# Kernel tuning notes

Measured on AMD Instinct MI355X. Metric: run time of the kernel, lower is better.

Reference implementation:

```python
import jax, jax.numpy as jnp
import numpy as np

N = 100000      # nodes
D = 128         # input feature dim
K = 8           # propagation hops (concat K+1 blocks)
HID = 512
OUT = 32
E = 1600000     # edges (avg degree 16)
BN_EPS = 1e-5
DEG_EPS = 1e-8


def setup_inputs() -> dict:
    key = jax.random.key(0)
    ks = jax.random.split(key, 8)
    feature = jax.random.normal(ks[0], (N, D), dtype=jnp.float32)
    coor = jax.random.uniform(ks[1], (N, 2), dtype=jnp.float32)
    edge_index = jax.random.randint(ks[2], (2, E), 0, N, dtype=jnp.int32)
    theta = jnp.array(1.0, dtype=jnp.float32)  # Gaussian bandwidth param
    fan1 = D * (K + 1)
    W1 = jax.random.normal(ks[3], (HID, fan1), dtype=jnp.float32) * (1.0 / np.sqrt(fan1))
    b1 = jnp.zeros((HID,), dtype=jnp.float32)
    gamma = jnp.ones((HID,), dtype=jnp.float32)
    beta = jnp.zeros((HID,), dtype=jnp.float32)
    W2 = jax.random.normal(ks[4], (OUT, HID), dtype=jnp.float32) * (1.0 / np.sqrt(HID))
    b2 = jnp.zeros((OUT,), dtype=jnp.float32)
    return {"feature": feature, "coor": coor, "theta": theta,
            "W1": W1, "b1": b1, "gamma": gamma, "beta": beta,
            "W2": W2, "b2": b2, "edge_index": edge_index, "m": 1}


def reference(feature, coor, theta, W1, b1, gamma, beta, W2, b2, edge_index, m):
    row, col = edge_index[0], edge_index[1]  # dst, src
    # Gaussian kernel edge weights from coordinate distances (gather on coor)
    diff = coor[row] - coor[col]                       # [E, 2]
    dist2 = jnp.sum(diff * diff, axis=-1)              # [E]
    w = jnp.exp(-dist2 * theta / m)                    # [E]
    # degree (row) normalization via scatter-add
    deg = jax.ops.segment_sum(w, row, num_segments=N)  # [N]
    norm = w / (deg[row] + DEG_EPS)                    # [E]
    # K sequential propagations, concat with input (-> N x D*(K+1))
    xs = [feature]
    x = feature
    for _ in range(K):
        msgs = x[col] * norm[:, None]                  # [E, D] gather + weight
        x = jax.ops.segment_sum(msgs, row, num_segments=N)  # [N, D] scatter
        xs.append(x)
    h = jnp.concatenate(xs, axis=-1)                   # [N, D*(K+1)]
    # MLP head: fc1 -> leaky_relu(0.2) -> BatchNorm1d (batch stats) -> fc2
    h = jax.nn.leaky_relu(h @ W1.T + b1, negative_slope=0.2)
    mu = jnp.mean(h, axis=0)
    var = jnp.var(h, axis=0)
    h = (h - mu) * jax.lax.rsqrt(var + BN_EPS) * gamma + beta
    # dropout omitted (deterministic/eval reference)
    return h @ W2.T + b2
```

## Files before the change

kernel.cpp:

```cpp
#include <hip/hip_runtime.h>
#include <hip/hip_bf16.h>
#include <cstdint>
#include <cstddef>

#define NNODES 100000
#define DFEAT 128
#define KHOP 8
#define FAN1 1152
#define HIDN 512
#define OUTD 32
#define NEDGE 1600000
#define BN_EPS 1e-5f
#define DEG_EPS 1e-8f

using short8 = __attribute__((ext_vector_type(8))) short;
using f32x4  = __attribute__((ext_vector_type(4))) float;

__device__ __forceinline__ float bf16lo(uint32_t u) { return __uint_as_float(u << 16); }
__device__ __forceinline__ float bf16hi(uint32_t u) { return __uint_as_float(u & 0xffff0000u); }
__device__ __forceinline__ float bf16s(short x) {
    return __uint_as_float(((uint32_t)(uint16_t)x) << 16);
}
__device__ __forceinline__ uint32_t packbf(float a, float b) {
    uint32_t lo = __bfloat16_as_ushort(__float2bfloat16(a));
    uint32_t hi = __bfloat16_as_ushort(__float2bfloat16(b));
    return lo | (hi << 16);
}

__device__ __forceinline__ void gload16(const void* g, void* l) {
    __builtin_amdgcn_global_load_lds(
        (const __attribute__((address_space(1))) uint32_t*)g,
        (__attribute__((address_space(3))) uint32_t*)l, 16, 0, 0);
}

struct Blk3 { const __hip_bfloat16* p[3]; };

__global__ __launch_bounds__(256) void edge_kernel(
    const int* __restrict__ ei, const float* __restrict__ coor,
    const float* __restrict__ theta, const int* __restrict__ mm,
    float* __restrict__ deg, int* __restrict__ cnt)
{
    int e = blockIdx.x * 256 + threadIdx.x;
    if (e >= NEDGE) return;
    float tom = theta[0] / (float)mm[0];
    int r = ei[e], c = ei[NEDGE + e];
    float2 pr = *(const float2*)(coor + 2*(size_t)r);
    float2 pc = *(const float2*)(coor + 2*(size_t)c);
    float dx = pr.x - pc.x, dy = pr.y - pc.y;
    float w = expf(-(dx*dx + dy*dy) * tom);
    atomicAdd(&deg[r], w);
    atomicAdd(&cnt[r], 1);
}

__global__ __launch_bounds__(1024) void scan_local(
    const int* __restrict__ cnt, int* __restrict__ row_ptr,
    int* __restrict__ bsum, int n)
{
    __shared__ int wsum[16];
    int b = blockIdx.x, tid = threadIdx.x;
    int i = b * 1024 + tid;
    int lane = tid & 63, wv = tid >> 6;
    int v = (i < n) ? cnt[i] : 0;
    #pragma unroll
    for (int off = 1; off < 64; off <<= 1) {
        int t = __shfl_up(v, off, 64);
        if (lane >= off) v += t;
    }
    if (lane == 63) wsum[wv] = v;
    __syncthreads();
    if (tid < 16) {
        int t = wsum[tid];
        #pragma unroll
        for (int off = 1; off < 16; off <<= 1) {
            int u = __shfl_up(t, off, 64);
            if (tid >= off) t += u;
        }
        wsum[tid] = t;
    }
    __syncthreads();
    int incl = v + ((wv == 0) ? 0 : wsum[wv - 1]);
    if (i < n) row_ptr[i + 1] = incl;
    if (tid == 0) bsum[b] = wsum[15];
}

__global__ __launch_bounds__(128) void scan_carry(int* __restrict__ bsum, int n)
{
    __shared__ int ws[2];
    int tid = threadIdx.x, lane = tid & 63, wv = tid >> 6;
    int v = (tid < n) ? bsum[tid] : 0;
    int incl = v;
    #pragma unroll
    for (int off = 1; off < 64; off <<= 1) {
        int t = __shfl_up(incl, off, 64);
        if (lane >= off) incl += t;
    }
    if (lane == 63) ws[wv] = incl;
    __syncthreads();
    int excl = incl - v + ((wv == 0) ? 0 : ws[0]);
    if (tid < n) bsum[tid] = excl;
}

__global__ __launch_bounds__(256) void scan_add(
    const int* __restrict__ bsum, int* __restrict__ row_ptr, int n)
{
    int i = blockIdx.x * 256 + threadIdx.x;
    if (i == 0) row_ptr[0] = 0;
    if (i < n) row_ptr[i + 1] += bsum[i >> 10];
}

__global__ __launch_bounds__(256) void fill_kernel(
    const int* __restrict__ ei, const float* __restrict__ coor,
    const float* __restrict__ theta, const int* __restrict__ mm,
    const float* __restrict__ deg, const int* __restrict__ row_ptr,
    int* __restrict__ fill, int* __restrict__ cols, float* __restrict__ nrm)
{
    int e = blockIdx.x * 256 + threadIdx.x;
    if (e >= NEDGE) return;
    float tom = theta[0] / (float)mm[0];
    int r = ei[e], c = ei[NEDGE + e];
    float2 pr = *(const float2*)(coor + 2*(size_t)r);
    float2 pc = *(const float2*)(coor + 2*(size_t)c);
    float dx = pr.x - pc.x, dy = pr.y - pc.y;
    float w = expf(-(dx*dx + dy*dy) * tom);
    int pos = row_ptr[r] + atomicAdd(&fill[r], 1);
    cols[pos] = c;
    nrm[pos] = w / (deg[r] + DEG_EPS);
}

__global__ __launch_bounds__(256) void cast_feat_kernel(
    const float* __restrict__ f, __hip_bfloat16* __restrict__ x0)
{
    int i = blockIdx.x * 256 + threadIdx.x;
    int node = i >> 6, l2 = i & 63;
    if (node >= NNODES) return;
    float2 v = *(const float2*)(f + (size_t)node * DFEAT + l2 * 2);
    __hip_bfloat162 hb;
    hb.x = __float2bfloat16(v.x);
    hb.y = __float2bfloat16(v.y);
    *(__hip_bfloat162*)(x0 + (size_t)node * DFEAT + l2 * 2) = hb;
}

__global__ __launch_bounds__(256) void cast_w1_kernel(
    const float* __restrict__ w1, __hip_bfloat16* __restrict__ o)
{
    int i = blockIdx.x * 256 + threadIdx.x;
    if (i < HIDN * FAN1) o[i] = __float2bfloat16(w1[i]);
}

__global__ __launch_bounds__(256) void prop_kernel(
    const __hip_bfloat16* __restrict__ x, __hip_bfloat16* __restrict__ y,
    const int* __restrict__ row_ptr, const int* __restrict__ cols,
    const float* __restrict__ nrm)
{
    int gw = (blockIdx.x * 256 + threadIdx.x) >> 6;
    if (gw >= NNODES) return;
    int lane = threadIdx.x & 63;
    int q = lane >> 4, sl = lane & 15;
    int beg = row_ptr[gw], end = row_ptr[gw + 1];
    float a0 = 0.f, a1 = 0.f, a2 = 0.f, a3 = 0.f;
    float a4 = 0.f, a5 = 0.f, a6 = 0.f, a7 = 0.f;
    int e = beg + q;
    for (; e + 12 < end; e += 16) {
        int s0 = cols[e], s1 = cols[e + 4], s2 = cols[e + 8], s3 = cols[e + 12];
        float w0 = nrm[e], w1 = nrm[e + 4], w2 = nrm[e + 8], w3 = nrm[e + 12];
        uint4 u0 = *(const uint4*)(x + (size_t)s0 * DFEAT + sl * 8);
        uint4 u1 = *(const uint4*)(x + (size_t)s1 * DFEAT + sl * 8);
        uint4 u2 = *(const uint4*)(x + (size_t)s2 * DFEAT + sl * 8);
        uint4 u3 = *(const uint4*)(x + (size_t)s3 * DFEAT + sl * 8);
        a0 += w0 * bf16lo(u0.x); a1 += w0 * bf16hi(u0.x);
        a2 += w0 * bf16lo(u0.y); a3 += w0 * bf16hi(u0.y);
        a4 += w0 * bf16lo(u0.z); a5 += w0 * bf16hi(u0.z);
        a6 += w0 * bf16lo(u0.w); a7 += w0 * bf16hi(u0.w);
        a0 += w1 * bf16lo(u1.x); a1 += w1 * bf16hi(u1.x);
        a2 += w1 * bf16lo(u1.y); a3 += w1 * bf16hi(u1.y);
        a4 += w1 * bf16lo(u1.z); a5 += w1 * bf16hi(u1.z);
        a6 += w1 * bf16lo(u1.w); a7 += w1 * bf16hi(u1.w);
        a0 += w2 * bf16lo(u2.x); a1 += w2 * bf16hi(u2.x);
        a2 += w2 * bf16lo(u2.y); a3 += w2 * bf16hi(u2.y);
        a4 += w2 * bf16lo(u2.z); a5 += w2 * bf16hi(u2.z);
        a6 += w2 * bf16lo(u2.w); a7 += w2 * bf16hi(u2.w);
        a0 += w3 * bf16lo(u3.x); a1 += w3 * bf16hi(u3.x);
        a2 += w3 * bf16lo(u3.y); a3 += w3 * bf16hi(u3.y);
        a4 += w3 * bf16lo(u3.z); a5 += w3 * bf16hi(u3.z);
        a6 += w3 * bf16lo(u3.w); a7 += w3 * bf16hi(u3.w);
    }
    for (; e < end; e += 4) {
        int s0 = cols[e];
        float w0 = nrm[e];
        uint4 u0 = *(const uint4*)(x + (size_t)s0 * DFEAT + sl * 8);
        a0 += w0 * bf16lo(u0.x); a1 += w0 * bf16hi(u0.x);
        a2 += w0 * bf16lo(u0.y); a3 += w0 * bf16hi(u0.y);
        a4 += w0 * bf16lo(u0.z); a5 += w0 * bf16hi(u0.z);
        a6 += w0 * bf16lo(u0.w); a7 += w0 * bf16hi(u0.w);
    }
    a0 += __shfl_xor(a0, 16, 64); a0 += __shfl_xor(a0, 32, 64);
    a1 += __shfl_xor(a1, 16, 64); a1 += __shfl_xor(a1, 32, 64);
    a2 += __shfl_xor(a2, 16, 64); a2 += __shfl_xor(a2, 32, 64);
    a3 += __shfl_xor(a3, 16, 64); a3 += __shfl_xor(a3, 32, 64);
    a4 += __shfl_xor(a4, 16, 64); a4 += __shfl_xor(a4, 32, 64);
    a5 += __shfl_xor(a5, 16, 64); a5 += __shfl_xor(a5, 32, 64);
    a6 += __shfl_xor(a6, 16, 64); a6 += __shfl_xor(a6, 32, 64);
    a7 += __shfl_xor(a7, 16, 64); a7 += __shfl_xor(a7, 32, 64);
    if (q == 0) {
        uint4 o;
        o.x = packbf(a0, a1);
        o.y = packbf(a2, a3);
        o.z = packbf(a4, a5);
        o.w = packbf(a6, a7);
        *(uint4*)(y + (size_t)gw * DFEAT + sl * 8) = o;
    }
}

__global__ __launch_bounds__(256) void fc1_kernel(
    Blk3 blks, const __hip_bfloat16* __restrict__ w1,
    const float* __restrict__ b1, __hip_bfloat16* __restrict__ h1b,
    float* __restrict__ gsum, float* __restrict__ gsq,
    int nkt, int kb0, int mode)
{
    __shared__ char smem[33792];
    int pid = blockIdx.x;
    int lid = (pid & 7) * 391 + (pid >> 3);
    int n0 = (lid & 3) * 128;
    int m0 = (lid >> 2) * 128;
    int tid = threadIdx.x, lane = tid & 63, wv = tid >> 6;
    int wr = wv >> 1, wc = wv & 1;

    f32x4 acc[4][4];
    #pragma unroll
    for (int i = 0; i < 4; ++i)
        #pragma unroll
        for (int j = 0; j < 4; ++j)
            acc[i][j] = (f32x4){0.f, 0.f, 0.f, 0.f};

#define STAGE(hb, ktv) do {                                                   \
        const __hip_bfloat16* xp = blks.p[(ktv) >> 2];                        \
        int koff_ = ((ktv) & 3) * 32;                                         \
        int kglob_ = (kb0 + ((ktv) >> 2)) * 128 + koff_;                      \
        char* Ab_ = smem + (hb) * 16384;                                      \
        char* Bb_ = Ab_ + 8192;                                               \
        _Pragma("unroll")                                                     \
        for (int l = 0; l < 2; ++l) {                                         \
            int u = l * 256 + wv * 64 + lane;                                 \
            int row_ = u >> 2, qq_ = u & 3;                                   \
            gload16(xp + (size_t)(m0 + row_) * DFEAT + koff_ + qq_ * 8,       \
                    Ab_ + u * 16);                                            \
            gload16(w1 + (size_t)(n0 + row_) * FAN1 + kglob_ + qq_ * 8,       \
                    Bb_ + u * 16);                                            \
        }                                                                     \
    } while (0)

    STAGE(0, 0);
    for (int kt = 0; kt < nkt; ++kt) {
        int cur = kt & 1;
        __builtin_amdgcn_s_barrier();
        if (kt + 1 < nkt) {
            STAGE(cur ^ 1, kt + 1);
            asm volatile("s_waitcnt vmcnt(4)" ::: "memory");
        } else {
            asm volatile("s_waitcnt vmcnt(0)" ::: "memory");
        }
        __builtin_amdgcn_s_barrier();
        char* Ab = smem + cur * 16384;
        char* Bb = Ab + 8192;
        short8 af[4], bfr[4];
        #pragma unroll
        for (int i = 0; i < 4; ++i)
            af[i] = *(const short8*)(Ab + (wr * 64 + i * 16 + (lane & 15)) * 64 + (lane >> 4) * 16);
        #pragma unroll
        for (int j = 0; j < 4; ++j)
            bfr[j] = *(const short8*)(Bb + (wc * 64 + j * 16 + (lane & 15)) * 64 + (lane >> 4) * 16);
        #pragma unroll
        for (int j = 0; j < 4; ++j)
            #pragma unroll
            for (int i = 0; i < 4; ++i)
                acc[i][j] = __builtin_amdgcn_mfma_f32_16x16x32_bf16(af[i], bfr[j], acc[i][j], 0, 0, 0);
    }
#undef STAGE

    __syncthreads();
    __hip_bfloat16* tile = (__hip_bfloat16*)smem;
    float* lsum = (float*)(smem + 32768);
    float* lsq  = lsum + 128;
    bool fin = (mode & 2) != 0;
    if (fin && tid < 128) { lsum[tid] = 0.f; lsq[tid] = 0.f; }
    #pragma unroll
    for (int i = 0; i < 4; ++i) {
        #pragma unroll
        for (int j = 0; j < 4; ++j) {
            int col = wc * 64 + j * 16 + (lane & 15);
            #pragma unroll
            for (int r = 0; r < 4; ++r) {
                int row = wr * 64 + i * 16 + (lane >> 4) * 4 + r;
                tile[row * 128 + col] = __float2bfloat16(acc[i][j][r]);
            }
        }
    }
    __syncthreads();

    int cu = tid & 15, tr = tid >> 4;
    float bias[8];
    float s[8], q[8];
    #pragma unroll
    for (int e = 0; e < 8; ++e) { s[e] = 0.f; q[e] = 0.f; }
    if (fin) {
        #pragma unroll
        for (int e = 0; e < 8; ++e) bias[e] = b1[n0 + cu * 8 + e];
    }
    size_t blkbase = (size_t)(n0 >> 7) * NNODES * 128;
    for (int p = 0; p < 8; ++p) {
        int row = p * 16 + tr;
        int gm = m0 + row;
        if (gm >= NNODES) continue;
        short8 fresh = *(const short8*)(tile + row * 128 + cu * 8);
        size_t gidx = blkbase + (size_t)gm * 128 + cu * 8;
        float v[8];
        #pragma unroll
        for (int e = 0; e < 8; ++e) v[e] = bf16s(fresh[e]);
        if (mode & 1) {
            short8 prev = *(const short8*)(h1b + gidx);
            #pragma unroll
            for (int e = 0; e < 8; ++e) v[e] += bf16s(prev[e]);
        }
        if (fin) {
            #pragma unroll
            for (int e = 0; e < 8; ++e) {
                float t = v[e] + bias[e];
                t = (t > 0.f) ? t : 0.2f * t;
                v[e] = t;
                s[e] += t;
                q[e] += t * t;
            }
        }
        short8 outv;
        #pragma unroll
        for (int e = 0; e < 8; ++e) outv[e] = (short)__bfloat16_as_ushort(__float2bfloat16(v[e]));
        *(short8*)(h1b + gidx) = outv;
    }
    if (fin) {
        #pragma unroll
        for (int e = 0; e < 8; ++e) {
            atomicAdd(&lsum[cu * 8 + e], s[e]);
            atomicAdd(&lsq[cu * 8 + e], q[e]);
        }
        __syncthreads();
        if (tid < 128) {
            atomicAdd(&gsum[n0 + tid], lsum[tid]);
            atomicAdd(&gsq[n0 + tid], lsq[tid]);
        }
    }
}

__global__ __launch_bounds__(512) void bn_finalize(
    const float* __restrict__ gsum, const float* __restrict__ gsq,
    const float* __restrict__ gamma, const float* __restrict__ beta,
    const float* __restrict__ w2, const float* __restrict__ b2,
    __hip_bfloat16* __restrict__ w2s, float* __restrict__ cvec)
{
    __shared__ float ts[HIDN];
    int tid = threadIdx.x;
    float mu = gsum[tid] * (1.0f / NNODES);
    float var = gsq[tid] * (1.0f / NNODES) - mu * mu;
    float s = gamma[tid] * rsqrtf(var + BN_EPS);
    float t = beta[tid] - mu * s;
    ts[tid] = t;
    for (int o = 0; o < OUTD; ++o)
        w2s[o * HIDN + tid] = __float2bfloat16(w2[o * HIDN + tid] * s);
    __syncthreads();
    int lane = tid & 63, wv = tid >> 6;
    for (int o = wv; o < OUTD; o += 8) {
        float p = 0.f;
        for (int j = lane; j < HIDN; j += 64) p += ts[j] * w2[o * HIDN + j];
        #pragma unroll
        for (int off = 32; off; off >>= 1) p += __shfl_xor(p, off, 64);
        if (lane == 0) cvec[o] = p + b2[o];
    }
}

__global__ __launch_bounds__(256) void fc2_kernel(
    const __hip_bfloat16* __restrict__ h1b, const __hip_bfloat16* __restrict__ w2s,
    const float* __restrict__ cvec, float* __restrict__ out)
{
    int gw = (blockIdx.x * 256 + threadIdx.x) >> 6;
    if (gw >= NNODES / 16) return;
    int lane = threadIdx.x & 63;
    int m0 = gw * 16;
    f32x4 acc[2];
    acc[0] = (f32x4){0.f, 0.f, 0.f, 0.f};
    acc[1] = (f32x4){0.f, 0.f, 0.f, 0.f};
    #pragma unroll
    for (int kt = 0; kt < HIDN / 32; ++kt) {
        int k0 = kt * 32;
        short8 a = *(const short8*)(h1b
            + ((size_t)(kt >> 2) * NNODES + (m0 + (lane & 15))) * 128
            + (kt & 3) * 32 + (lane >> 4) * 8);
        #pragma unroll
        for (int j = 0; j < 2; ++j) {
            short8 b = *(const short8*)(w2s + (size_t)(j * 16 + (lane & 15)) * HIDN + k0 + (lane >> 4) * 8);
            acc[j] = __builtin_amdgcn_mfma_f32_16x16x32_bf16(a, b, acc[j], 0, 0, 0);
        }
    }
    #pragma unroll
    for (int j = 0; j < 2; ++j) {
        int col = j * 16 + (lane & 15);
        float cadd = cvec[col];
        #pragma unroll
        for (int r = 0; r < 4; ++r) {
            int row = m0 + (lane >> 4) * 4 + r;
            out[(size_t)row * OUTD + col] = acc[j][r] + cadd;
        }
    }
}

struct Ptrs {
    float *deg, *nrm, *gsum, *gsq, *cvec;
    int *cnt, *fillc, *row_ptr, *colsb, *bsum;
    __hip_bfloat16 *slot[3], *h1acc, *w1b, *w2s;
};

static size_t layout(char* base, Ptrs& P) {
    char* p = base;
    auto take = [&](size_t b) {
        char* q = (char*)(((uintptr_t)p + 255) & ~(uintptr_t)255);
        p = q + b;
        return q;
    };
    P.deg     = (float*)take((size_t)NNODES * 4);
    P.cnt     = (int*)  take((size_t)NNODES * 4);
    P.fillc   = (int*)  take((size_t)NNODES * 4);
    P.row_ptr = (int*)  take((size_t)(NNODES + 1) * 4);
    P.bsum    = (int*)  take(128 * 4);
    P.colsb   = (int*)  take((size_t)NEDGE * 4);
    P.nrm     = (float*)take((size_t)NEDGE * 4);
    P.h1acc   = (__hip_bfloat16*)take((size_t)NNODES * HIDN * 2 + 65536);
    P.w1b     = (__hip_bfloat16*)take((size_t)HIDN * FAN1 * 2);
    P.w2s     = (__hip_bfloat16*)take((size_t)OUTD * HIDN * 2);
    P.gsum    = (float*)take(HIDN * 4);
    P.gsq     = (float*)take(HIDN * 4);
    P.cvec    = (float*)take(OUTD * 4);
    for (int i = 0; i < 3; ++i)
        P.slot[i] = (__hip_bfloat16*)take((size_t)NNODES * DFEAT * 2 + 32768);
    return (size_t)(p - base);
}

extern "C" void kernel_launch(void* const* d_in, const int* in_sizes, int n_in,
                              void* d_out, int out_size, void* d_ws, size_t ws_size,
                              hipStream_t stream)
{
    const float* feature = (const float*)d_in[0];
    const float* coor    = (const float*)d_in[1];
    const float* theta   = (const float*)d_in[2];
    const float* W1      = (const float*)d_in[3];
    const float* b1      = (const float*)d_in[4];
    const float* gamma   = (const float*)d_in[5];
    const float* beta    = (const float*)d_in[6];
    const float* W2      = (const float*)d_in[7];
    const float* b2      = (const float*)d_in[8];
    const int*   ei      = (const int*)d_in[9];
    const int*   mm      = (const int*)d_in[10];
    float* out = (float*)d_out;
    (void)in_sizes; (void)n_in; (void)out_size; (void)ws_size;

    Ptrs P;
    layout((char*)d_ws, P);

    hipMemsetAsync(P.deg,   0, (size_t)NNODES * 4, stream);
    hipMemsetAsync(P.cnt,   0, (size_t)NNODES * 4, stream);
    hipMemsetAsync(P.fillc, 0, (size_t)NNODES * 4, stream);
    hipMemsetAsync(P.gsum,  0, HIDN * 4, stream);
    hipMemsetAsync(P.gsq,   0, HIDN * 4, stream);

    int eb = (NEDGE + 255) / 256;
    int nchunk = (NNODES + 1023) / 1024;
    edge_kernel<<<eb, 256, 0, stream>>>(ei, coor, theta, mm, P.deg, P.cnt);
    scan_local<<<nchunk, 1024, 0, stream>>>(P.cnt, P.row_ptr, P.bsum, NNODES);
    scan_carry<<<1, 128, 0, stream>>>(P.bsum, nchunk);
    scan_add<<<(NNODES + 255) / 256, 256, 0, stream>>>(P.bsum, P.row_ptr, NNODES);
    fill_kernel<<<eb, 256, 0, stream>>>(ei, coor, theta, mm, P.deg, P.row_ptr,
                                        P.fillc, P.colsb, P.nrm);

    cast_w1_kernel<<<(HIDN * FAN1 + 255) / 256, 256, 0, stream>>>(W1, P.w1b);
    cast_feat_kernel<<<(NNODES * 64) / 256, 256, 0, stream>>>(feature, P.slot[0]);

    int pb = (NNODES * 64) / 256;
    int fgrid = 8 * 391;

    auto launch_fc1 = [&](int kb0, int mode) {
        Blk3 b;
        for (int i = 0; i < 3; ++i) b.p[i] = P.slot[i];
        fc1_kernel<<<fgrid, 256, 0, stream>>>(b, P.w1b, b1, P.h1acc,
                                              P.gsum, P.gsq, 12, kb0, mode);
    };

    for (int k = 1; k <= KHOP; ++k) {
        prop_kernel<<<pb, 256, 0, stream>>>(P.slot[(k - 1) % 3],
                                            P.slot[k % 3],
                                            P.row_ptr, P.colsb, P.nrm);
        if (k == 2) launch_fc1(0, 0);
        if (k == 5) launch_fc1(3, 1);
    }
    launch_fc1(6, 3);

    bn_finalize<<<1, 512, 0, stream>>>(P.gsum, P.gsq, gamma, beta, W2, b2,
                                       P.w2s, P.cvec);
    fc2_kernel<<<(NNODES / 16 * 64 + 255) / 256, 256, 0, stream>>>(P.h1acc, P.w2s,
                                                                   P.cvec, out);
}
```

Measured before the change: 1.030 ms.

## Pack degree and count into one 64-bit atomic, record per-edge rank, interleave CSR edges

The separate float degree and int count atomics are merged into a single 64-bit atomicAdd that holds a fixed-point weight sum in the low 48 bits and the edge count in the high bits. The returned old count becomes a per-edge rank, so the fill pass no longer needs a second atomic counter or its memset. Column index and normalized weight are stored interleaved as a uint2, so the propagation kernel issues one 8-byte load per edge instead of two 4-byte loads. In exchange, degree becomes fixed-point (2^26 scale), which loses some precision, and the 16-bit rank assumes no node has more than 65535 in-edges.

```diff
diff --git a/kernel.cpp b/kernel.cpp
--- a/kernel.cpp
+++ b/kernel.cpp
@@ -12,6 +12,7 @@
 #define NEDGE 1600000
 #define BN_EPS 1e-5f
 #define DEG_EPS 1e-8f
+#define FIXSCALE 67108864.0f
 
 using short8 = __attribute__((ext_vector_type(8))) short;
 using f32x4  = __attribute__((ext_vector_type(4))) float;
@@ -38,7 +39,7 @@
 __global__ __launch_bounds__(256) void edge_kernel(
     const int* __restrict__ ei, const float* __restrict__ coor,
     const float* __restrict__ theta, const int* __restrict__ mm,
-    float* __restrict__ deg, int* __restrict__ cnt)
+    unsigned long long* __restrict__ packed, unsigned short* __restrict__ rank)
 {
     int e = blockIdx.x * 256 + threadIdx.x;
     if (e >= NEDGE) return;
@@ -48,19 +49,21 @@
     float2 pc = *(const float2*)(coor + 2*(size_t)c);
     float dx = pr.x - pc.x, dy = pr.y - pc.y;
     float w = expf(-(dx*dx + dy*dy) * tom);
-    atomicAdd(&deg[r], w);
-    atomicAdd(&cnt[r], 1);
+    unsigned long long enc = (1ULL << 48)
+        | (unsigned long long)(unsigned int)__float2uint_rn(w * FIXSCALE);
+    unsigned long long old = atomicAdd(&packed[r], enc);
+    rank[e] = (unsigned short)(old >> 48);
 }
 
 __global__ __launch_bounds__(1024) void scan_local(
-    const int* __restrict__ cnt, int* __restrict__ row_ptr,
+    const unsigned long long* __restrict__ packed, int* __restrict__ row_ptr,
     int* __restrict__ bsum, int n)
 {
     __shared__ int wsum[16];
     int b = blockIdx.x, tid = threadIdx.x;
     int i = b * 1024 + tid;
     int lane = tid & 63, wv = tid >> 6;
-    int v = (i < n) ? cnt[i] : 0;
+    int v = (i < n) ? (int)(packed[i] >> 48) : 0;
     #pragma unroll
     for (int off = 1; off < 64; off <<= 1) {
         int t = __shfl_up(v, off, 64);
@@ -111,8 +114,9 @@
 __global__ __launch_bounds__(256) void fill_kernel(
     const int* __restrict__ ei, const float* __restrict__ coor,
     const float* __restrict__ theta, const int* __restrict__ mm,
-    const float* __restrict__ deg, const int* __restrict__ row_ptr,
-    int* __restrict__ fill, int* __restrict__ cols, float* __restrict__ nrm)
+    const unsigned long long* __restrict__ packed,
+    const unsigned short* __restrict__ rank, const int* __restrict__ row_ptr,
+    uint2* __restrict__ edat)
 {
     int e = blockIdx.x * 256 + threadIdx.x;
     if (e >= NEDGE) return;
@@ -122,9 +126,12 @@
     float2 pc = *(const float2*)(coor + 2*(size_t)c);
     float dx = pr.x - pc.x, dy = pr.y - pc.y;
     float w = expf(-(dx*dx + dy*dy) * tom);
-    int pos = row_ptr[r] + atomicAdd(&fill[r], 1);
-    cols[pos] = c;
-    nrm[pos] = w / (deg[r] + DEG_EPS);
+    float deg = (float)(double)(packed[r] & 0xFFFFFFFFFFFFULL) * (1.0f / FIXSCALE);
+    int pos = row_ptr[r] + rank[e];
+    uint2 d;
+    d.x = (unsigned)c;
+    d.y = __float_as_uint(w / (deg + DEG_EPS));
+    edat[pos] = d;
 }
 
 __global__ __launch_bounds__(256) void cast_feat_kernel(
@@ -149,8 +156,7 @@
 
 __global__ __launch_bounds__(256) void prop_kernel(
     const __hip_bfloat16* __restrict__ x, __hip_bfloat16* __restrict__ y,
-    const int* __restrict__ row_ptr, const int* __restrict__ cols,
-    const float* __restrict__ nrm)
+    const int* __restrict__ row_ptr, const uint2* __restrict__ edat)
 {
     int gw = (blockIdx.x * 256 + threadIdx.x) >> 6;
     if (gw >= NNODES) return;
@@ -161,12 +167,13 @@
     float a4 = 0.f, a5 = 0.f, a6 = 0.f, a7 = 0.f;
     int e = beg + q;
     for (; e + 12 < end; e += 16) {
-        int s0 = cols[e], s1 = cols[e + 4], s2 = cols[e + 8], s3 = cols[e + 12];
-        float w0 = nrm[e], w1 = nrm[e + 4], w2 = nrm[e + 8], w3 = nrm[e + 12];
-        uint4 u0 = *(const uint4*)(x + (size_t)s0 * DFEAT + sl * 8);
-        uint4 u1 = *(const uint4*)(x + (size_t)s1 * DFEAT + sl * 8);
-        uint4 u2 = *(const uint4*)(x + (size_t)s2 * DFEAT + sl * 8);
-        uint4 u3 = *(const uint4*)(x + (size_t)s3 * DFEAT + sl * 8);
+        uint2 e0 = edat[e], e1 = edat[e + 4], e2 = edat[e + 8], e3 = edat[e + 12];
+        float w0 = __uint_as_float(e0.y), w1 = __uint_as_float(e1.y);
+        float w2 = __uint_as_float(e2.y), w3 = __uint_as_float(e3.y);
+        uint4 u0 = *(const uint4*)(x + (size_t)e0.x * DFEAT + sl * 8);
+        uint4 u1 = *(const uint4*)(x + (size_t)e1.x * DFEAT + sl * 8);
+        uint4 u2 = *(const uint4*)(x + (size_t)e2.x * DFEAT + sl * 8);
+        uint4 u3 = *(const uint4*)(x + (size_t)e3.x * DFEAT + sl * 8);
         a0 += w0 * bf16lo(u0.x); a1 += w0 * bf16hi(u0.x);
         a2 += w0 * bf16lo(u0.y); a3 += w0 * bf16hi(u0.y);
         a4 += w0 * bf16lo(u0.z); a5 += w0 * bf16hi(u0.z);
@@ -185,9 +192,9 @@
         a6 += w3 * bf16lo(u3.w); a7 += w3 * bf16hi(u3.w);
     }
     for (; e < end; e += 4) {
-        int s0 = cols[e];
-        float w0 = nrm[e];
-        uint4 u0 = *(const uint4*)(x + (size_t)s0 * DFEAT + sl * 8);
+        uint2 e0 = edat[e];
+        float w0 = __uint_as_float(e0.y);
+        uint4 u0 = *(const uint4*)(x + (size_t)e0.x * DFEAT + sl * 8);
         a0 += w0 * bf16lo(u0.x); a1 += w0 * bf16hi(u0.x);
         a2 += w0 * bf16lo(u0.y); a3 += w0 * bf16hi(u0.y);
         a4 += w0 * bf16lo(u0.z); a5 += w0 * bf16hi(u0.z);
@@ -412,8 +419,11 @@
 }
 
 struct Ptrs {
-    float *deg, *nrm, *gsum, *gsq, *cvec;
-    int *cnt, *fillc, *row_ptr, *colsb, *bsum;
+    float *gsum, *gsq, *cvec;
+    int *row_ptr, *bsum;
+    unsigned long long* packed;
+    unsigned short* rank;
+    uint2* edat;
     __hip_bfloat16 *slot[3], *h1acc, *w1b, *w2s;
 };
 
@@ -424,13 +434,11 @@
         p = q + b;
         return q;
     };
-    P.deg     = (float*)take((size_t)NNODES * 4);
-    P.cnt     = (int*)  take((size_t)NNODES * 4);
-    P.fillc   = (int*)  take((size_t)NNODES * 4);
+    P.packed  = (unsigned long long*)take((size_t)NNODES * 8);
+    P.rank    = (unsigned short*)take((size_t)NEDGE * 2);
     P.row_ptr = (int*)  take((size_t)(NNODES + 1) * 4);
     P.bsum    = (int*)  take(128 * 4);
-    P.colsb   = (int*)  take((size_t)NEDGE * 4);
-    P.nrm     = (float*)take((size_t)NEDGE * 4);
+    P.edat    = (uint2*)take((size_t)NEDGE * 8);
     P.h1acc   = (__hip_bfloat16*)take((size_t)NNODES * HIDN * 2 + 65536);
     P.w1b     = (__hip_bfloat16*)take((size_t)HIDN * FAN1 * 2);
     P.w2s     = (__hip_bfloat16*)take((size_t)OUTD * HIDN * 2);
@@ -463,20 +471,18 @@
     Ptrs P;
     layout((char*)d_ws, P);
 
-    hipMemsetAsync(P.deg,   0, (size_t)NNODES * 4, stream);
-    hipMemsetAsync(P.cnt,   0, (size_t)NNODES * 4, stream);
-    hipMemsetAsync(P.fillc, 0, (size_t)NNODES * 4, stream);
-    hipMemsetAsync(P.gsum,  0, HIDN * 4, stream);
-    hipMemsetAsync(P.gsq,   0, HIDN * 4, stream);
+    hipMemsetAsync(P.packed, 0, (size_t)NNODES * 8, stream);
+    hipMemsetAsync(P.gsum,   0, HIDN * 4, stream);
+    hipMemsetAsync(P.gsq,    0, HIDN * 4, stream);
 
     int eb = (NEDGE + 255) / 256;
     int nchunk = (NNODES + 1023) / 1024;
-    edge_kernel<<<eb, 256, 0, stream>>>(ei, coor, theta, mm, P.deg, P.cnt);
-    scan_local<<<nchunk, 1024, 0, stream>>>(P.cnt, P.row_ptr, P.bsum, NNODES);
+    edge_kernel<<<eb, 256, 0, stream>>>(ei, coor, theta, mm, P.packed, P.rank);
+    scan_local<<<nchunk, 1024, 0, stream>>>(P.packed, P.row_ptr, P.bsum, NNODES);
     scan_carry<<<1, 128, 0, stream>>>(P.bsum, nchunk);
     scan_add<<<(NNODES + 255) / 256, 256, 0, stream>>>(P.bsum, P.row_ptr, NNODES);
-    fill_kernel<<<eb, 256, 0, stream>>>(ei, coor, theta, mm, P.deg, P.row_ptr,
-                                        P.fillc, P.colsb, P.nrm);
+    fill_kernel<<<eb, 256, 0, stream>>>(ei, coor, theta, mm, P.packed, P.rank,
+                                        P.row_ptr, P.edat);
 
     cast_w1_kernel<<<(HIDN * FAN1 + 255) / 256, 256, 0, stream>>>(W1, P.w1b);
     cast_feat_kernel<<<(NNODES * 64) / 256, 256, 0, stream>>>(feature, P.slot[0]);
@@ -494,7 +500,7 @@
     for (int k = 1; k <= KHOP; ++k) {
         prop_kernel<<<pb, 256, 0, stream>>>(P.slot[(k - 1) % 3],
                                             P.slot[k % 3],
-                                            P.row_ptr, P.colsb, P.nrm);
+                                            P.row_ptr, P.edat);
         if (k == 2) launch_fc1(0, 0);
         if (k == 5) launch_fc1(3, 1);
     }
```

Result: faster. 924.1 us (-10.3%).
